# Kernel tuning notes

Measured on AMD Instinct MI355X. Metric: run time of the kernel, lower is better.

The kernel has to match this reference:

```python
import jax, jax.numpy as jnp
import numpy as np

N, K, D = 262144, 1024, 64

def setup_inputs() -> dict:
    key = jax.random.key(0)
    kx, kc = jax.random.split(key)
    x = jax.random.normal(kx, (N, D), dtype=jnp.float32)
    centers = jax.random.normal(kc, (K, D), dtype=jnp.float32)
    return {"x": x, "centers": centers}

def reference(x, centers):
    # centers_norm is precomputed as a buffer in the torch module: (centers**2).sum(-1)
    centers_norm = jnp.sum(centers * centers, axis=-1)           # [K]
    x_norm = jnp.sum(x * x, axis=-1)                             # [N]
    dist = x_norm[..., None] - 2.0 * (x @ centers.T) + centers_norm  # [N,K]
    return jnp.argmin(jnp.abs(dist), axis=-1)                    # [N] int ids
```

## Files before the change

kernel.cpp:

```cpp
#include <hip/hip_runtime.h>
#include <float.h>


#define N_PTS 262144
#define K_CTR 1024
#define DIM   64
#define CTILE 64
#define NTILE (K_CTR / CTILE)
#define OFFC  32.0f
#define TAU_DIST 0.05f

#define WS_CN    0
#define WS_CI    4096
#define WS_HI    8192
#define WS_LO    139264
#define WS_CTR   270336
#define WS_LIST  270592
#define WS_MIN   (270592 + 4 * 65536)

typedef __attribute__((ext_vector_type(8))) short  short8;
typedef __attribute__((ext_vector_type(8))) __bf16 bf16x8;
typedef __attribute__((ext_vector_type(4))) float  f32x4;

union FragU { short8 s; bf16x8 b; unsigned short u[8]; };

static __device__ __forceinline__ unsigned short bfbits(__bf16 h) {
    return __builtin_bit_cast(unsigned short, h);
}

#if defined(__has_builtin)
#if __has_builtin(__builtin_amdgcn_global_load_lds)
#define HAVE_GLD 1
#endif
#endif

#ifdef HAVE_GLD
#define GLD16(gsrc, ldst)                                                      \
    __builtin_amdgcn_global_load_lds(                                          \
        (const __attribute__((address_space(1))) void*)(gsrc),                 \
        (__attribute__((address_space(3))) void*)(ldst), 16, 0, 0)
#endif

__global__ void prep_kernel(const float* __restrict__ centers,
                            float* __restrict__ cn, float* __restrict__ ci,
                            int* __restrict__ counter) {
    int k = blockIdx.x * 256 + threadIdx.x;
    if (k == 0) *counter = 0;
    if (k < K_CTR) {
        const float4* c = reinterpret_cast<const float4*>(centers + (size_t)k * DIM);
        float s0 = 0.f, s1 = 0.f, s2 = 0.f, s3 = 0.f;
#pragma unroll
        for (int j = 0; j < 16; ++j) {
            float4 v = c[j];
            s0 = fmaf(v.x, v.x, s0); s1 = fmaf(v.y, v.y, s1);
            s2 = fmaf(v.z, v.z, s2); s3 = fmaf(v.w, v.w, s3);
        }
        float n = (s0 + s1) + (s2 + s3);
        cn[k] = n;
        ci[k] = fmaf(-0.5f, n, -OFFC);
    }
}

__global__ void split_kernel(const float* __restrict__ centers,
                             unsigned short* __restrict__ hiG,
                             unsigned short* __restrict__ loG) {
    int si = blockIdx.x * 256 + threadIdx.x;
    int lane = si & 63, ks = (si >> 6) & 1, st = (si >> 7) & 3, tile = si >> 9;
    int row = tile * CTILE + st * 16 + (lane & 15);
    int dimb = ks * 32 + ((lane >> 4) & 3) * 8;
    const float* g = centers + (size_t)row * DIM + dimb;
    float4 v0 = *reinterpret_cast<const float4*>(g);
    float4 v1 = *reinterpret_cast<const float4*>(g + 4);
    float vv[8] = {v0.x, v0.y, v0.z, v0.w, v1.x, v1.y, v1.z, v1.w};
    FragU hi, lo;
#pragma unroll
    for (int j = 0; j < 8; ++j) {
        __bf16 h = (__bf16)vv[j];
        hi.u[j] = bfbits(h);
        lo.u[j] = bfbits((__bf16)(vv[j] - (float)h));
    }
    *reinterpret_cast<short8*>(hiG + (size_t)si * 8) = hi.s;
    *reinterpret_cast<short8*>(loG + (size_t)si * 8) = lo.s;
}

__launch_bounds__(256, 2)
__global__ void assign_mfma(const float* __restrict__ x,
                            const unsigned short* __restrict__ hiG,
                            const unsigned short* __restrict__ loG,
                            const float* __restrict__ ci,
                            int* __restrict__ out,
                            int* __restrict__ counter,
                            int* __restrict__ list, int cap) {
    __shared__ __align__(16) unsigned short lh[2 * 512 * 8];
    __shared__ __align__(16) unsigned short ll[2 * 512 * 8];
    __shared__ __align__(16) float ciL[K_CTR];

    const int tid  = threadIdx.x;
    const int wv   = tid >> 6;
    const int lane = tid & 63;
    const int g    = lane >> 4;
    const int lr   = lane & 15;
    const int pbase = blockIdx.x * 256 + wv * 64;

#pragma unroll
    for (int j = 0; j < 4; ++j) ciL[j * 256 + tid] = ci[j * 256 + tid];

    bf16x8 bh[4][2], bl[4][2];
#pragma unroll
    for (int cb = 0; cb < 4; ++cb) {
        const int p = pbase + cb * 16 + lr;
        const float* xr = x + (size_t)p * DIM + g * 8;
        float4 v0 = *reinterpret_cast<const float4*>(xr);
        float4 v1 = *reinterpret_cast<const float4*>(xr + 4);
        float4 v2 = *reinterpret_cast<const float4*>(xr + 32);
        float4 v3 = *reinterpret_cast<const float4*>(xr + 36);
        float vv[16] = {v0.x, v0.y, v0.z, v0.w, v1.x, v1.y, v1.z, v1.w,
                        v2.x, v2.y, v2.z, v2.w, v3.x, v3.y, v3.z, v3.w};
#pragma unroll
        for (int j = 0; j < 16; ++j) {
            __bf16 hb = (__bf16)vv[j];
            bh[cb][j >> 3][j & 7] = hb;
            bl[cb][j >> 3][j & 7] = (__bf16)(vv[j] - (float)hb);
        }
    }

    unsigned int best[4], sec[4];
#pragma unroll
    for (int cb = 0; cb < 4; ++cb) { best[cb] = 0xFFFFFFFFu; sec[cb] = 0xFFFFFFFFu; }

#define STAGE(buf, tile)                                                       \
    do {                                                                       \
        const size_t sb = (size_t)((tile) * 512 + wv * 64 + lane) * 8;         \
        unsigned short* dh = lh + ((buf) * 512 + wv * 64) * 8;                 \
        unsigned short* dl = ll + ((buf) * 512 + wv * 64) * 8;                 \
        GLD16(hiG + sb, dh);                                                   \
        GLD16(hiG + sb + 256 * 8, dh + 256 * 8);                               \
        GLD16(loG + sb, dl);                                                   \
        GLD16(loG + sb + 256 * 8, dl + 256 * 8);                               \
    } while (0)

#ifndef HAVE_GLD
#undef STAGE
#define STAGE(buf, tile)                                                       \
    do {                                                                       \
        const short8* hs = reinterpret_cast<const short8*>(hiG) + (tile) * 512; \
        const short8* ls = reinterpret_cast<const short8*>(loG) + (tile) * 512; \
        short8* hd = reinterpret_cast<short8*>(lh) + (buf) * 512;              \
        short8* ld = reinterpret_cast<short8*>(ll) + (buf) * 512;              \
        hd[tid] = hs[tid]; hd[256 + tid] = hs[256 + tid];                      \
        ld[tid] = ls[tid]; ld[256 + tid] = ls[256 + tid];                      \
    } while (0)
#endif

    STAGE(0, 0);
    __syncthreads();

    int cur = 0;
#pragma unroll 1
    for (int tile = 0; tile < NTILE; ++tile) {
        if (tile < NTILE - 1) STAGE(cur ^ 1, tile + 1);

        const char* lhc = (const char*)lh + cur * 512 * 16 + lane * 16;
        const char* llc = (const char*)ll + cur * 512 * 16 + lane * 16;
        const unsigned int ibt = tile * CTILE + g * 4;
        const float* cib = ciL + tile * CTILE + g * 4;

#pragma unroll
        for (int st = 0; st < CTILE / 16; ++st) {
            FragU ah0, ah1, al0, al1;
            ah0.s = *reinterpret_cast<const short8*>(lhc + st * 2048);
            ah1.s = *reinterpret_cast<const short8*>(lhc + st * 2048 + 1024);
            al0.s = *reinterpret_cast<const short8*>(llc + st * 2048);
            al1.s = *reinterpret_cast<const short8*>(llc + st * 2048 + 1024);
            const f32x4 init4 = *reinterpret_cast<const f32x4*>(cib + st * 16);

            f32x4 acc[4];
            __builtin_amdgcn_s_setprio(1);
#pragma unroll
            for (int cb = 0; cb < 4; ++cb)
                acc[cb] = __builtin_amdgcn_mfma_f32_16x16x32_bf16(ah0.b, bh[cb][0], init4, 0, 0, 0);
#pragma unroll
            for (int cb = 0; cb < 4; ++cb)
                acc[cb] = __builtin_amdgcn_mfma_f32_16x16x32_bf16(ah0.b, bl[cb][0], acc[cb], 0, 0, 0);
#pragma unroll
            for (int cb = 0; cb < 4; ++cb)
                acc[cb] = __builtin_amdgcn_mfma_f32_16x16x32_bf16(al0.b, bh[cb][0], acc[cb], 0, 0, 0);
#pragma unroll
            for (int cb = 0; cb < 4; ++cb)
                acc[cb] = __builtin_amdgcn_mfma_f32_16x16x32_bf16(ah1.b, bh[cb][1], acc[cb], 0, 0, 0);
#pragma unroll
            for (int cb = 0; cb < 4; ++cb)
                acc[cb] = __builtin_amdgcn_mfma_f32_16x16x32_bf16(ah1.b, bl[cb][1], acc[cb], 0, 0, 0);
#pragma unroll
            for (int cb = 0; cb < 4; ++cb)
                acc[cb] = __builtin_amdgcn_mfma_f32_16x16x32_bf16(al1.b, bh[cb][1], acc[cb], 0, 0, 0);
            __builtin_amdgcn_s_setprio(0);

            unsigned int vidx[4];
            vidx[0] = ibt + st * 16;
            vidx[1] = vidx[0] + 1; vidx[2] = vidx[0] + 2; vidx[3] = vidx[0] + 3;

#pragma unroll
            for (int cb = 0; cb < 4; ++cb) {
#pragma unroll
                for (int pr = 0; pr < 2; ++pr) {
                    unsigned int ka = (__float_as_uint(acc[cb][pr * 2 + 0]) & 0xFFFFFC00u) | vidx[pr * 2 + 0];
                    unsigned int kb = (__float_as_uint(acc[cb][pr * 2 + 1]) & 0xFFFFFC00u) | vidx[pr * 2 + 1];
                    unsigned int bo = best[cb], med, bn;
                    asm("v_med3_u32 %0, %1, %2, %3" : "=v"(med) : "v"(ka), "v"(kb), "v"(bo));
                    asm("v_min3_u32 %0, %1, %2, %3" : "=v"(bn)  : "v"(ka), "v"(kb), "v"(bo));
                    best[cb] = bn;
                    sec[cb]  = min(sec[cb], med);
                }
            }
        }

        __syncthreads();
        cur ^= 1;
    }

#pragma unroll
    for (int cb = 0; cb < 4; ++cb) {
        unsigned int b = best[cb], s = sec[cb];
#pragma unroll
        for (int off = 16; off <= 32; off <<= 1) {
            unsigned int ob = __shfl_xor(b, off);
            unsigned int os = __shfl_xor(s, off);
            s = min(min(s, os), max(b, ob));
            b = min(b, ob);
        }
        if (g == 0) {
            const int p = pbase + cb * 16 + lr;
            out[p] = (int)(b & 1023u);
            float bf = __uint_as_float(b & 0xFFFFFC00u);
            float sf = __uint_as_float(s & 0xFFFFFC00u);
            if ((b < 0x80000000u) || (2.f * (bf - sf) < TAU_DIST)) {
                int sl = atomicAdd(counter, 1);
                if (sl < cap) list[sl] = p;
            }
        }
    }
}

__launch_bounds__(256, 2)
__global__ void refine2_kernel(const float* __restrict__ x,
                               const float* __restrict__ centers,
                               const float* __restrict__ cn,
                               const int* __restrict__ list,
                               const int* __restrict__ counter,
                               int* __restrict__ out, int cap) {
    __shared__ float ldsC[64 * 65];
    int cnt = *counter; if (cnt > cap) cnt = cap;
    const int tid  = threadIdx.x;
    const int wv   = tid >> 6;
    const int lane = tid & 63;

#pragma unroll 1
    for (int base = blockIdx.x * 4; base < cnt; base += gridDim.x * 4) {
        const int i = base + wv;
        const bool valid = (i < cnt);
        const int p = valid ? list[i] : 0;

        const float4* xr = reinterpret_cast<const float4*>(x + (size_t)p * DIM);
        float4 xv[16];
        float xn0 = 0.f, xn1 = 0.f, xn2 = 0.f, xn3 = 0.f;
#pragma unroll
        for (int j = 0; j < 16; ++j) {
            float4 v = xr[j]; xv[j] = v;
            xn0 = fmaf(v.x, v.x, xn0); xn1 = fmaf(v.y, v.y, xn1);
            xn2 = fmaf(v.z, v.z, xn2); xn3 = fmaf(v.w, v.w, xn3);
        }
        const float xnv = (xn0 + xn1) + (xn2 + xn3);

        float bestv = 3.4e38f; int bi = 0;
#pragma unroll 1
        for (int t = 0; t < 16; ++t) {
            __syncthreads();
#pragma unroll
            for (int j = 0; j < 16; ++j) {
                int idx = j * 256 + tid;
                int row = idx >> 6, col = idx & 63;
                ldsC[row * 65 + col] = centers[((size_t)t * 64 + row) * DIM + col];
            }
            __syncthreads();
            if (valid) {
                const int k = t * 64 + lane;
                const float* cr = ldsC + lane * 65;
                float a0 = 0.f, a1 = 0.f, a2 = 0.f, a3 = 0.f;
#pragma unroll
                for (int jj = 0; jj < 16; ++jj) {
                    a0 = fmaf(xv[jj].x, cr[jj * 4 + 0], a0);
                    a1 = fmaf(xv[jj].y, cr[jj * 4 + 1], a1);
                    a2 = fmaf(xv[jj].z, cr[jj * 4 + 2], a2);
                    a3 = fmaf(xv[jj].w, cr[jj * 4 + 3], a3);
                }
                float dot  = (a0 + a1) + (a2 + a3);
                float dist = fabsf(fmaf(-2.f, dot, xnv + cn[k]));
                if (dist < bestv) { bestv = dist; bi = k; }
            }
        }
#pragma unroll
        for (int off = 1; off < 64; off <<= 1) {
            float ob = __shfl_xor(bestv, off);
            int   oi = __shfl_xor(bi, off);
            bool take = (ob < bestv) || (ob == bestv && oi < bi);
            bestv = take ? ob : bestv;
            bi    = take ? oi : bi;
        }
        if (valid && lane == 0) out[p] = bi;
    }
}

#define TK 128
__launch_bounds__(256, 4)
__global__ void assign_fp32(const float* __restrict__ x,
                            const float* __restrict__ centers,
                            const float* __restrict__ cn,
                            int* __restrict__ out) {
    __shared__ float ldsC[TK * DIM];
    __shared__ float ldsN[TK];
    const int tid = threadIdx.x;
    const int p = blockIdx.x * 256 + tid;
    const float4* xr = reinterpret_cast<const float4*>(x + (size_t)p * DIM);
    float4 xv[16];
    float xn0 = 0.f, xn1 = 0.f, xn2 = 0.f, xn3 = 0.f;
#pragma unroll
    for (int j = 0; j < 16; ++j) {
        float4 v = xr[j]; xv[j] = v;
        xn0 = fmaf(v.x, v.x, xn0); xn1 = fmaf(v.y, v.y, xn1);
        xn2 = fmaf(v.z, v.z, xn2); xn3 = fmaf(v.w, v.w, xn3);
    }
    const float xn = (xn0 + xn1) + (xn2 + xn3);
    float bestv = 3.4e38f; int best = 0;
#pragma unroll 1
    for (int t = 0; t < K_CTR / TK; ++t) {
        __syncthreads();
        const float4* cg = reinterpret_cast<const float4*>(centers + (size_t)t * TK * DIM);
        float4* cl = reinterpret_cast<float4*>(ldsC);
#pragma unroll
        for (int j = 0; j < (TK * DIM / 4) / 256; ++j)
            cl[j * 256 + tid] = cg[j * 256 + tid];
        if (tid < TK) ldsN[tid] = cn[t * TK + tid];
        __syncthreads();
        for (int k = 0; k < TK; ++k) {
            const float4* cv = reinterpret_cast<const float4*>(ldsC + k * DIM);
            float a0 = 0.f, a1 = 0.f, a2 = 0.f, a3 = 0.f;
#pragma unroll
            for (int j = 0; j < 16; ++j) {
                float4 c4 = cv[j];
                a0 = fmaf(xv[j].x, c4.x, a0); a1 = fmaf(xv[j].y, c4.y, a1);
                a2 = fmaf(xv[j].z, c4.z, a2); a3 = fmaf(xv[j].w, c4.w, a3);
            }
            float dot = (a0 + a1) + (a2 + a3);
            float dist = fabsf(fmaf(-2.f, dot, xn + ldsN[k]));
            if (dist < bestv) { bestv = dist; best = t * TK + k; }
        }
    }
    out[p] = best;
}

extern "C" void kernel_launch(void* const* d_in, const int* in_sizes, int n_in,
                              void* d_out, int out_size, void* d_ws, size_t ws_size,
                              hipStream_t stream) {
    const float* x = (const float*)d_in[0];
    const float* centers = (const float*)d_in[1];
    int* out = (int*)d_out;
    char* ws = (char*)d_ws;
    float* cn = (float*)(ws + WS_CN);
    float* ci = (float*)(ws + WS_CI);
    unsigned short* hiG = (unsigned short*)(ws + WS_HI);
    unsigned short* loG = (unsigned short*)(ws + WS_LO);
    int* counter = (int*)(ws + WS_CTR);
    int* list = (int*)(ws + WS_LIST);

    if (ws_size >= WS_MIN) {
        size_t avail = (ws_size - WS_LIST) / sizeof(int);
        int cap = (int)(avail < (size_t)N_PTS ? avail : (size_t)N_PTS);
        prep_kernel<<<4, 256, 0, stream>>>(centers, cn, ci, counter);
        split_kernel<<<32, 256, 0, stream>>>(centers, hiG, loG);
        assign_mfma<<<N_PTS / 256, 256, 0, stream>>>(x, hiG, loG, ci, out, counter, list, cap);
        refine2_kernel<<<1024, 256, 0, stream>>>(x, centers, cn, list, counter, out, cap);
    } else {
        prep_kernel<<<4, 256, 0, stream>>>(centers, cn, ci, counter);
        assign_fp32<<<N_PTS / 256, 256, 0, stream>>>(x, centers, cn, out);
    }
}
```

Baseline: 118.1 us.

## Switch distance MFMA from 16x16x32 to 32x32x16 bf16 tiles

Reorganizes the split-bf16 distance GEMM to use 32x32x16 MFMA instructions. Each wave now covers 32 centers by 32 points per instruction, with matching changes to the center fragment packing, the per-lane x fragments and the epilogue reduction. Larger MFMA tiles cut the number of instructions and LDS fragment loads per FLOP, and the cross-lane shuffle reduction shrinks to one step. The trade-off is a larger accumulator (16 floats per tile), which raises register pressure at the requested occupancy of 2 blocks.

After: 132.2 us. +12.0%, slower.

```diff
diff --git a/kernel.cpp b/kernel.cpp
--- a/kernel.cpp
+++ b/kernel.cpp
@@ -18,9 +18,10 @@
 #define WS_LIST  270592
 #define WS_MIN   (270592 + 4 * 65536)
 
-typedef __attribute__((ext_vector_type(8))) short  short8;
-typedef __attribute__((ext_vector_type(8))) __bf16 bf16x8;
-typedef __attribute__((ext_vector_type(4))) float  f32x4;
+typedef __attribute__((ext_vector_type(8)))  short  short8;
+typedef __attribute__((ext_vector_type(8)))  __bf16 bf16x8;
+typedef __attribute__((ext_vector_type(4)))  float  f32x4;
+typedef __attribute__((ext_vector_type(16))) float  f32x16;
 
 union FragU { short8 s; bf16x8 b; unsigned short u[8]; };
 
@@ -65,9 +66,9 @@
                              unsigned short* __restrict__ hiG,
                              unsigned short* __restrict__ loG) {
     int si = blockIdx.x * 256 + threadIdx.x;
-    int lane = si & 63, ks = (si >> 6) & 1, st = (si >> 7) & 3, tile = si >> 9;
-    int row = tile * CTILE + st * 16 + (lane & 15);
-    int dimb = ks * 32 + ((lane >> 4) & 3) * 8;
+    int lane = si & 63, ks = (si >> 6) & 3, ct = si >> 8;
+    int row = ct * 32 + (lane & 31);
+    int dimb = ks * 16 + ((lane >> 5) & 1) * 8;
     const float* g = centers + (size_t)row * DIM + dimb;
     float4 v0 = *reinterpret_cast<const float4*>(g);
     float4 v1 = *reinterpret_cast<const float4*>(g + 4);
@@ -98,35 +99,36 @@
     const int tid  = threadIdx.x;
     const int wv   = tid >> 6;
     const int lane = tid & 63;
-    const int g    = lane >> 4;
-    const int lr   = lane & 15;
+    const int col  = lane & 31;
+    const int khalf = lane >> 5;
+    const int hi4  = khalf * 4;
     const int pbase = blockIdx.x * 256 + wv * 64;
 
 #pragma unroll
     for (int j = 0; j < 4; ++j) ciL[j * 256 + tid] = ci[j * 256 + tid];
 
-    bf16x8 bh[4][2], bl[4][2];
-#pragma unroll
-    for (int cb = 0; cb < 4; ++cb) {
-        const int p = pbase + cb * 16 + lr;
-        const float* xr = x + (size_t)p * DIM + g * 8;
-        float4 v0 = *reinterpret_cast<const float4*>(xr);
-        float4 v1 = *reinterpret_cast<const float4*>(xr + 4);
-        float4 v2 = *reinterpret_cast<const float4*>(xr + 32);
-        float4 v3 = *reinterpret_cast<const float4*>(xr + 36);
-        float vv[16] = {v0.x, v0.y, v0.z, v0.w, v1.x, v1.y, v1.z, v1.w,
-                        v2.x, v2.y, v2.z, v2.w, v3.x, v3.y, v3.z, v3.w};
-#pragma unroll
-        for (int j = 0; j < 16; ++j) {
-            __bf16 hb = (__bf16)vv[j];
-            bh[cb][j >> 3][j & 7] = hb;
-            bl[cb][j >> 3][j & 7] = (__bf16)(vv[j] - (float)hb);
-        }
-    }
-
-    unsigned int best[4], sec[4];
-#pragma unroll
-    for (int cb = 0; cb < 4; ++cb) { best[cb] = 0xFFFFFFFFu; sec[cb] = 0xFFFFFFFFu; }
+    bf16x8 bh[2][4], bl[2][4];
+#pragma unroll
+    for (int pb = 0; pb < 2; ++pb) {
+        const int p = pbase + pb * 32 + col;
+        const float* xr = x + (size_t)p * DIM + khalf * 8;
+#pragma unroll
+        for (int ks = 0; ks < 4; ++ks) {
+            float4 v0 = *reinterpret_cast<const float4*>(xr + ks * 16);
+            float4 v1 = *reinterpret_cast<const float4*>(xr + ks * 16 + 4);
+            float vv[8] = {v0.x, v0.y, v0.z, v0.w, v1.x, v1.y, v1.z, v1.w};
+#pragma unroll
+            for (int j = 0; j < 8; ++j) {
+                __bf16 hb = (__bf16)vv[j];
+                bh[pb][ks][j] = hb;
+                bl[pb][ks][j] = (__bf16)(vv[j] - (float)hb);
+            }
+        }
+    }
+
+    unsigned int best[2], sec[2];
+#pragma unroll
+    for (int pb = 0; pb < 2; ++pb) { best[pb] = 0xFFFFFFFFu; sec[pb] = 0xFFFFFFFFu; }
 
 #define STAGE(buf, tile)                                                       \
     do {                                                                       \
@@ -160,57 +162,65 @@
     for (int tile = 0; tile < NTILE; ++tile) {
         if (tile < NTILE - 1) STAGE(cur ^ 1, tile + 1);
 
-        const char* lhc = (const char*)lh + cur * 512 * 16 + lane * 16;
-        const char* llc = (const char*)ll + cur * 512 * 16 + lane * 16;
-        const unsigned int ibt = tile * CTILE + g * 4;
-        const float* cib = ciL + tile * CTILE + g * 4;
-
-#pragma unroll
-        for (int st = 0; st < CTILE / 16; ++st) {
-            FragU ah0, ah1, al0, al1;
-            ah0.s = *reinterpret_cast<const short8*>(lhc + st * 2048);
-            ah1.s = *reinterpret_cast<const short8*>(lhc + st * 2048 + 1024);
-            al0.s = *reinterpret_cast<const short8*>(llc + st * 2048);
-            al1.s = *reinterpret_cast<const short8*>(llc + st * 2048 + 1024);
-            const f32x4 init4 = *reinterpret_cast<const f32x4*>(cib + st * 16);
-
-            f32x4 acc[4];
+        const char* lhb = (const char*)lh + cur * 8192 + lane * 16;
+        const char* llb = (const char*)ll + cur * 8192 + lane * 16;
+
+#pragma unroll
+        for (int gi = 0; gi < 2; ++gi) {
+            const int ctbase = tile * CTILE + gi * 32;
+
+            FragU Ah[4], Al[4];
+#pragma unroll
+            for (int ks = 0; ks < 4; ++ks) {
+                Ah[ks].s = *reinterpret_cast<const short8*>(lhb + gi * 4096 + ks * 1024);
+                Al[ks].s = *reinterpret_cast<const short8*>(llb + gi * 4096 + ks * 1024);
+            }
+
+            f32x16 init;
+#pragma unroll
+            for (int q = 0; q < 4; ++q) {
+                f32x4 iq = *reinterpret_cast<const f32x4*>(ciL + ctbase + q * 8 + hi4);
+#pragma unroll
+                for (int j = 0; j < 4; ++j) init[q * 4 + j] = iq[j];
+            }
+
+            f32x16 acc[2];
             __builtin_amdgcn_s_setprio(1);
 #pragma unroll
-            for (int cb = 0; cb < 4; ++cb)
-                acc[cb] = __builtin_amdgcn_mfma_f32_16x16x32_bf16(ah0.b, bh[cb][0], init4, 0, 0, 0);
-#pragma unroll
-            for (int cb = 0; cb < 4; ++cb)
-                acc[cb] = __builtin_amdgcn_mfma_f32_16x16x32_bf16(ah0.b, bl[cb][0], acc[cb], 0, 0, 0);
-#pragma unroll
-            for (int cb = 0; cb < 4; ++cb)
-                acc[cb] = __builtin_amdgcn_mfma_f32_16x16x32_bf16(al0.b, bh[cb][0], acc[cb], 0, 0, 0);
-#pragma unroll
-            for (int cb = 0; cb < 4; ++cb)
-                acc[cb] = __builtin_amdgcn_mfma_f32_16x16x32_bf16(ah1.b, bh[cb][1], acc[cb], 0, 0, 0);
-#pragma unroll
-            for (int cb = 0; cb < 4; ++cb)
-                acc[cb] = __builtin_amdgcn_mfma_f32_16x16x32_bf16(ah1.b, bl[cb][1], acc[cb], 0, 0, 0);
-#pragma unroll
-            for (int cb = 0; cb < 4; ++cb)
-                acc[cb] = __builtin_amdgcn_mfma_f32_16x16x32_bf16(al1.b, bh[cb][1], acc[cb], 0, 0, 0);
+            for (int pb = 0; pb < 2; ++pb)
+                acc[pb] = __builtin_amdgcn_mfma_f32_32x32x16_bf16(Ah[0].b, bh[pb][0], init, 0, 0, 0);
+#pragma unroll
+            for (int ks = 1; ks < 4; ++ks)
+#pragma unroll
+                for (int pb = 0; pb < 2; ++pb)
+                    acc[pb] = __builtin_amdgcn_mfma_f32_32x32x16_bf16(Ah[ks].b, bh[pb][ks], acc[pb], 0, 0, 0);
+#pragma unroll
+            for (int ks = 0; ks < 4; ++ks)
+#pragma unroll
+                for (int pb = 0; pb < 2; ++pb)
+                    acc[pb] = __builtin_amdgcn_mfma_f32_32x32x16_bf16(Ah[ks].b, bl[pb][ks], acc[pb], 0, 0, 0);
+#pragma unroll
+            for (int ks = 0; ks < 4; ++ks)
+#pragma unroll
+                for (int pb = 0; pb < 2; ++pb)
+                    acc[pb] = __builtin_amdgcn_mfma_f32_32x32x16_bf16(Al[ks].b, bh[pb][ks], acc[pb], 0, 0, 0);
             __builtin_amdgcn_s_setprio(0);
 
-            unsigned int vidx[4];
-            vidx[0] = ibt + st * 16;
-            vidx[1] = vidx[0] + 1; vidx[2] = vidx[0] + 2; vidx[3] = vidx[0] + 3;
-
-#pragma unroll
-            for (int cb = 0; cb < 4; ++cb) {
-#pragma unroll
-                for (int pr = 0; pr < 2; ++pr) {
-                    unsigned int ka = (__float_as_uint(acc[cb][pr * 2 + 0]) & 0xFFFFFC00u) | vidx[pr * 2 + 0];
-                    unsigned int kb = (__float_as_uint(acc[cb][pr * 2 + 1]) & 0xFFFFFC00u) | vidx[pr * 2 + 1];
-                    unsigned int bo = best[cb], med, bn;
-                    asm("v_med3_u32 %0, %1, %2, %3" : "=v"(med) : "v"(ka), "v"(kb), "v"(bo));
-                    asm("v_min3_u32 %0, %1, %2, %3" : "=v"(bn)  : "v"(ka), "v"(kb), "v"(bo));
-                    best[cb] = bn;
-                    sec[cb]  = min(sec[cb], med);
+#pragma unroll
+            for (int pb = 0; pb < 2; ++pb) {
+#pragma unroll
+                for (int q = 0; q < 4; ++q) {
+                    const unsigned int kb0 = (unsigned int)(ctbase + q * 8 + hi4);
+#pragma unroll
+                    for (int pr = 0; pr < 2; ++pr) {
+                        unsigned int ka = (__float_as_uint(acc[pb][q * 4 + pr * 2 + 0]) & 0xFFFFFC00u) | (kb0 + pr * 2 + 0);
+                        unsigned int kb = (__float_as_uint(acc[pb][q * 4 + pr * 2 + 1]) & 0xFFFFFC00u) | (kb0 + pr * 2 + 1);
+                        unsigned int bo = best[pb], med, bn;
+                        asm("v_med3_u32 %0, %1, %2, %3" : "=v"(med) : "v"(ka), "v"(kb), "v"(bo));
+                        asm("v_min3_u32 %0, %1, %2, %3" : "=v"(bn)  : "v"(ka), "v"(kb), "v"(bo));
+                        best[pb] = bn;
+                        sec[pb]  = min(sec[pb], med);
+                    }
                 }
             }
         }
@@ -220,17 +230,14 @@
     }
 
 #pragma unroll
-    for (int cb = 0; cb < 4; ++cb) {
-        unsigned int b = best[cb], s = sec[cb];
-#pragma unroll
-        for (int off = 16; off <= 32; off <<= 1) {
-            unsigned int ob = __shfl_xor(b, off);
-            unsigned int os = __shfl_xor(s, off);
-            s = min(min(s, os), max(b, ob));
-            b = min(b, ob);
-        }
-        if (g == 0) {
-            const int p = pbase + cb * 16 + lr;
+    for (int pb = 0; pb < 2; ++pb) {
+        unsigned int b = best[pb], s = sec[pb];
+        unsigned int ob = __shfl_xor(b, 32);
+        unsigned int os = __shfl_xor(s, 32);
+        s = min(min(s, os), max(b, ob));
+        b = min(b, ob);
+        if (lane < 32) {
+            const int p = pbase + pb * 32 + lane;
             out[p] = (int)(b & 1023u);
             float bf = __uint_as_float(b & 0xFFFFFC00u);
             float sf = __uint_as_float(s & 0xFFFFFC00u);
```
